# Kernel tuning notes

Measured on AMD Instinct MI355X. Metric: run time of the kernel, lower is better.

Reference implementation:

```python
import jax, jax.numpy as jnp
import numpy as np

B, T, D = 32, 2048, 256
HOUT, K = 512, 8
H = HOUT // 2  # per-direction hidden


def _lstm(x, w_ih, w_hh, b_ih, b_hh):
    # x: [B,T,D]; torch gate order i,f,g,o
    b = x.shape[0]
    h0 = jnp.zeros((b, H), x.dtype)
    c0 = jnp.zeros((b, H), x.dtype)
    def step(carry, x_t):
        h, c = carry
        g = x_t @ w_ih.T + b_ih + h @ w_hh.T + b_hh
        i, f, gg, o = jnp.split(g, 4, axis=-1)
        c = jax.nn.sigmoid(f) * c + jax.nn.sigmoid(i) * jnp.tanh(gg)
        h = jax.nn.sigmoid(o) * jnp.tanh(c)
        return (h, c), h
    _, hs = jax.lax.scan(step, (h0, c0), jnp.swapaxes(x, 0, 1))
    return jnp.swapaxes(hs, 0, 1)  # [B,T,H]


def setup_inputs() -> dict:
    key = jax.random.key(0)
    ks = jax.random.split(key, 16)
    s = 0.1
    lengths = jax.random.randint(ks[1], (B,), T // 2, T + 1)
    mask = (jnp.arange(T)[None, :] < lengths[:, None])
    inp = {
        "sentences": jax.random.normal(ks[0], (B, T, D), jnp.float32),
        "tags": jax.random.randint(ks[2], (B, T), 0, K),
        "lengths": lengths,
        "mask": mask,
        # forward-direction LSTM params
        "w_ih_f": jax.random.normal(ks[3], (4 * H, D), jnp.float32) * s,
        "w_hh_f": jax.random.normal(ks[4], (4 * H, H), jnp.float32) * s,
        "b_ih_f": jax.random.normal(ks[5], (4 * H,), jnp.float32) * s,
        "b_hh_f": jax.random.normal(ks[6], (4 * H,), jnp.float32) * s,
        # backward-direction LSTM params
        "w_ih_b": jax.random.normal(ks[7], (4 * H, D), jnp.float32) * s,
        "w_hh_b": jax.random.normal(ks[8], (4 * H, H), jnp.float32) * s,
        "b_ih_b": jax.random.normal(ks[9], (4 * H,), jnp.float32) * s,
        "b_hh_b": jax.random.normal(ks[10], (4 * H,), jnp.float32) * s,
        # hidden2tag linear
        "w_tag": jax.random.normal(ks[11], (K, HOUT), jnp.float32) * s,
        "b_tag": jax.random.normal(ks[12], (K,), jnp.float32) * s,
        # CRF params
        "start_trans": jax.random.normal(ks[13], (K,), jnp.float32) * s,
        "end_trans": jax.random.normal(ks[14], (K,), jnp.float32) * s,
        "trans": jax.random.normal(ks[15], (K, K), jnp.float32) * s,
    }
    return inp


def reference(sentences, tags, lengths, mask,
              w_ih_f, w_hh_f, b_ih_f, b_hh_f,
              w_ih_b, w_hh_b, b_ih_b, b_hh_b,
              w_tag, b_tag, start_trans, end_trans, trans):
    # --- BiLSTM features (dropout is identity at eval) ---
    t_idx = jnp.arange(T)[None, :]
    L = lengths[:, None]
    rev = jnp.where(t_idx < L, L - 1 - t_idx, t_idx)  # per-sequence reversal (involution)
    x_rev = jnp.take_along_axis(sentences, rev[:, :, None], axis=1)
    h_f = _lstm(sentences, w_ih_f, w_hh_f, b_ih_f, b_hh_f)
    h_b = jnp.take_along_axis(_lstm(x_rev, w_ih_b, w_hh_b, b_ih_b, b_hh_b), rev[:, :, None], axis=1)
    feats = jnp.concatenate([h_f, h_b], axis=-1)  # [B,T,HOUT]
    emis = feats @ w_tag.T + b_tag  # [B,T,K]

    m = mask.astype(emis.dtype)
    # --- CRF numerator (gold path score) ---
    tags0 = tags[:, 0]
    num = start_trans[tags0] + jnp.take_along_axis(emis[:, 0], tags0[:, None], 1)[:, 0]
    emis_tag = jnp.take_along_axis(emis, tags[:, :, None], 2)[..., 0]  # [B,T]
    tr = trans[tags[:, :-1], tags[:, 1:]]  # [B,T-1]
    num = num + jnp.sum((tr + emis_tag[:, 1:]) * m[:, 1:], axis=1)
    last_tags = jnp.take_along_axis(tags, (lengths - 1)[:, None], 1)[:, 0]
    num = num + end_trans[last_tags]

    # --- CRF log-partition (forward algorithm, logsumexp recurrence) ---
    def step(score, inp):
        e_t, m_t = inp  # [B,K], [B]
        nxt = jax.nn.logsumexp(score[:, :, None] + trans[None] + e_t[:, None, :], axis=1)
        return jnp.where(m_t[:, None], nxt, score), None
    score0 = start_trans[None, :] + emis[:, 0]
    xs = (jnp.swapaxes(emis[:, 1:], 0, 1), jnp.swapaxes(mask[:, 1:], 0, 1))
    scoreT, _ = jax.lax.scan(step, score0, xs)
    logZ = jax.nn.logsumexp(scoreT + end_trans[None, :], axis=1)

    # reduction='mean' log-likelihood, loss = -llh
    return -jnp.mean(num - logZ)
```

## Files before the change

kernel.cpp:

```cpp
#include <hip/hip_runtime.h>


constexpr int T_ = 2048, D_ = 256, K_ = 8;

typedef __bf16 v8bf __attribute__((ext_vector_type(8)));
typedef float  v4f  __attribute__((ext_vector_type(4)));
typedef int    v8i  __attribute__((ext_vector_type(8)));
typedef unsigned int u32;
typedef unsigned long long u64;

union U64x4 { u64 q[4]; v8i v; };

__device__ __forceinline__ float sigm(float x) {
  return __builtin_amdgcn_rcpf(1.f + __expf(-x));
}
__device__ __forceinline__ float tanh_f(float x) {
  return 1.f - 2.f * __builtin_amdgcn_rcpf(__expf(2.f * x) + 1.f);
}

__device__ __forceinline__ u32 pk2bf(float a, float b) {
  union { __bf16 h[2]; u32 u; } x; x.h[0] = (__bf16)a; x.h[1] = (__bf16)b; return x.u;
}
__device__ __forceinline__ float lobf(u32 u) { union { u32 u; __bf16 h[2]; } x; x.u = u; return (float)x.h[0]; }
__device__ __forceinline__ float hibf(u32 u) { union { u32 u; __bf16 h[2]; } x; x.u = u; return (float)x.h[1]; }

__device__ __forceinline__ int gate_row(int mtg, int rr) {
  return (rr & 3) * 256 + 32 * (mtg >> 3) + 8 * (rr >> 2) + (mtg & 7);
}


__global__ __launch_bounds__(256) void prepack(
    const float* __restrict__ w_hh_f, const float* __restrict__ w_hh_b,
    const float* __restrict__ b_ih_f, const float* __restrict__ b_hh_f,
    const float* __restrict__ b_ih_b, const float* __restrict__ b_hh_b,
    const float* __restrict__ w_tag,
    u64* wh8, v8bf* wt16, float* biasp, u32* hstate_u, float* cstate)
{
  int gid = blockIdx.x * 256 + threadIdx.x;
  if (gid < 65536) {
    int lane = gid & 63, kt = (gid >> 6) & 7, mtg = (gid >> 9) & 63, d = gid >> 15;
    int rr = lane & 15, q = lane >> 4;
    const float* whh = d ? w_hh_b : w_hh_f;
    const float* src = whh + (size_t)gate_row(mtg, rr) * 256
                           + 128 * (kt >> 2) + 32 * q + 8 * (kt & 3);
    u32 lo = __builtin_amdgcn_cvt_pk_fp8_f32(src[0], src[1], 0, false);
    lo = __builtin_amdgcn_cvt_pk_fp8_f32(src[2], src[3], lo, true);
    u32 hi = __builtin_amdgcn_cvt_pk_fp8_f32(src[4], src[5], 0, false);
    hi = __builtin_amdgcn_cvt_pk_fp8_f32(src[6], src[7], hi, true);
    wh8[gid] = ((u64)hi << 32) | lo;
  } else if (gid < 66560) {
    int g = gid - 65536;
    int lane = g & 63, kt = (g >> 6) & 7, d = (g >> 9) & 1;
    int rr = lane & 15, q = lane >> 4;
    v8bf v;
    #pragma unroll
    for (int e = 0; e < 8; ++e)
      v[e] = (rr < 8) ? (__bf16)w_tag[(size_t)rr * 512 + d * 256 + 32 * kt + 8 * q + e]
                      : (__bf16)0.f;
    wt16[g] = v;
  } else if (gid < 68608) {
    int g = gid - 66560;
    int p = g & 1023, d = g >> 10;
    int gr = gate_row(p >> 4, p & 15);
    biasp[g] = (d ? b_ih_b[gr] + b_hh_b[gr] : b_ih_f[gr] + b_hh_f[gr]);
  } else if (gid < 76800) {
    hstate_u[gid - 68608] = 0u;
  } else if (gid < 93184) {
    cstate[gid - 76800] = 0.f;
  }
}

__global__ __launch_bounds__(1024) void fused_chunk(
    const float* __restrict__ sent, const int* __restrict__ lengths,
    const float* __restrict__ w_ih_f, const float* __restrict__ w_ih_b,
    const float* __restrict__ biasp,
    const u64* __restrict__ wh8, const v8bf* __restrict__ wt16,
    __bf16* __restrict__ hstate, float* __restrict__ cstate,
    __bf16* __restrict__ pre, __bf16* __restrict__ hbuf,
    __bf16* __restrict__ emisF, __bf16* __restrict__ emisB,
    int crec, int cpre, int cemis, int CT, int TT, int nch, int NPREB)
{
  __shared__ __align__(16) char smem[33792];

  if (blockIdx.x < 4) {
    if (crec < 0) return;
    const int s = blockIdx.x, d = s >> 1, bg = s & 1;
    const int tid = threadIdx.x, lane = tid & 63, w = tid >> 6;
    const int fm = lane & 15, q = lane >> 4;
    const int e4 = 32 * (w >> 1) + 8 * q + 4 * (w & 1);
    int Lmax = 0;
    for (int i = 0; i < 32; ++i) Lmax = max(Lmax, lengths[i]);
    const int t0 = crec * CT, t1 = t0 + CT;
    const int tend = min(t1, Lmax);

    unsigned char* h8l = (unsigned char*)smem;

    {
      uint2 hv = *(const uint2*)(hstate + (size_t)s * 4096 + fm * 256 + e4);
      u32 pk8 = __builtin_amdgcn_cvt_pk_fp8_f32(lobf(hv.x), hibf(hv.x), 0, false);
      pk8 = __builtin_amdgcn_cvt_pk_fp8_f32(lobf(hv.y), hibf(hv.y), pk8, true);
      *(u32*)&h8l[4352 + fm * 272 + e4] = pk8;
    }

    v8i afr0[4], afr1[4];
    #pragma unroll
    for (int mt = 0; mt < 4; ++mt) {
      int mtg = 4 * w + mt;
      U64x4 lo, hi;
      #pragma unroll
      for (int jj = 0; jj < 4; ++jj) {
        lo.q[jj] = wh8[((size_t)(d * 64 + mtg) * 8 + jj) * 64 + lane];
        hi.q[jj] = wh8[((size_t)(d * 64 + mtg) * 8 + 4 + jj) * 64 + lane];
      }
      afr0[mt] = lo.v; afr1[mt] = hi.v;
    }
    float c8[4];
    #pragma unroll
    for (int mt = 0; mt < 4; ++mt) c8[mt] = cstate[((size_t)s * 1024 + tid) * 4 + mt];

    const char* preBase = (const char*)pre + (size_t)(crec & 1) * CT * 131072;
    __bf16* hslot = hbuf + ((size_t)(crec & 1) * 2 + d) * CT * 8192;
    const char* pb0 = preBase + (((size_t)d * CT * 32 + (bg * 16 + fm)) * 1024
                                 + 16 * (4 * w) + 4 * q) * 2;

    uint2 pA[4];
    #pragma unroll
    for (int mt = 0; mt < 4; ++mt)
      pA[mt] = *(const uint2*)(pb0 + 32 * mt);

    for (int t = t0; t < tend; ++t) {
      asm volatile("s_waitcnt lgkmcnt(0)" ::: "memory");
      __builtin_amdgcn_s_barrier();

      const int pp = (t + 1) & 1;
      v8i b0 = *(const v8i*)&h8l[pp * 4352 + fm * 272 + 32 * q];
      v8i b1 = *(const v8i*)&h8l[pp * 4352 + fm * 272 + 128 + 32 * q];

      v4f acc[4], accb[4];
      #pragma unroll
      for (int mt = 0; mt < 4; ++mt) {
        acc[mt] = v4f{lobf(pA[mt].x), hibf(pA[mt].x), lobf(pA[mt].y), hibf(pA[mt].y)};
        accb[mt] = v4f{0.f, 0.f, 0.f, 0.f};
      }

      {
        int tn = min(t + 1, tend - 1);
        const char* pb = pb0 + (size_t)(tn - t0) * 65536;
        #pragma unroll
        for (int mt = 0; mt < 4; ++mt)
          pA[mt] = *(const uint2*)(pb + 32 * mt);
      }

      #pragma unroll
      for (int mt = 0; mt < 4; ++mt)
        acc[mt] = __builtin_amdgcn_mfma_scale_f32_16x16x128_f8f6f4(
            afr0[mt], b0, acc[mt], 0, 0, 0, 0x7f7f7f7f, 0, 0x7f7f7f7f);
      #pragma unroll
      for (int mt = 0; mt < 4; ++mt)
        accb[mt] = __builtin_amdgcn_mfma_scale_f32_16x16x128_f8f6f4(
            afr1[mt], b1, accb[mt], 0, 0, 0, 0x7f7f7f7f, 0, 0x7f7f7f7f);

      float hh[4];
      #pragma unroll
      for (int mt = 0; mt < 4; ++mt) {
        float gi = acc[mt][0] + accb[mt][0];
        float gf = acc[mt][1] + accb[mt][1];
        float gg = acc[mt][2] + accb[mt][2];
        float go = acc[mt][3] + accb[mt][3];
        float c = sigm(gf) * c8[mt] + sigm(gi) * tanh_f(gg);
        c8[mt] = c;
        hh[mt] = sigm(go) * tanh_f(c);
      }

      {
        u32 pk8 = __builtin_amdgcn_cvt_pk_fp8_f32(hh[0], hh[1], 0, false);
        pk8 = __builtin_amdgcn_cvt_pk_fp8_f32(hh[2], hh[3], pk8, true);
        *(u32*)&h8l[(t & 1) * 4352 + fm * 272 + e4] = pk8;
      }
      {
        uint2 hv;
        hv.x = pk2bf(hh[0], hh[1]); hv.y = pk2bf(hh[2], hh[3]);
        *(uint2*)(hslot + ((size_t)(t - t0) * 32 + bg * 16 + fm) * 256 + e4) = hv;
        if (t == tend - 1)
          *(uint2*)(hstate + (size_t)s * 4096 + fm * 256 + e4) = hv;
      }
    }

    if (tend > t0) {
      #pragma unroll
      for (int mt = 0; mt < 4; ++mt) cstate[((size_t)s * 1024 + tid) * 4 + mt] = c8[mt];
    }
    return;
  }

  if ((int)blockIdx.x < 4 + NPREB) {
    if (cpre >= nch) return;
    const bool act = threadIdx.x < 512;
    const int u = (blockIdx.x - 4) * 2 + (threadIdx.x >> 8);
    const int b = u & 31, d = (u >> 5) & 1, zz = u >> 6;
    const int tg = zz >> 2, rg = zz & 3;
    const int tid = threadIdx.x & 255, lane = tid & 63, w = tid >> 6;
    const int fm = lane & 15, q = lane >> 4;
    const int NT = TT >> 4;
    const int t0 = cpre * CT;
    const float* wih = d ? w_ih_b : w_ih_f;
    __bf16* xl = (__bf16*)(smem + (threadIdx.x >> 8) * 16896);
    __bf16* preS = pre + (size_t)(cpre & 1) * CT * 65536;

    if (act) {
      const int Lb = lengths[b];
      for (int rep = 0; rep < NT; ++rep) {
        int tl = (tid >> 4) + 16 * rep, c16 = (tid & 15) * 16;
        int tglob = t0 + TT * tg + tl;
        int pos = d ? ((tglob < Lb) ? (Lb - 1 - tglob) : tglob) : tglob;
        const float4* xp = (const float4*)(sent + ((size_t)b * T_ + pos) * D_ + c16);
        float4 a0 = xp[0], a1 = xp[1], a2 = xp[2], a3 = xp[3];
        v8bf v0, v1;
        v0[0]=(__bf16)a0.x; v0[1]=(__bf16)a0.y; v0[2]=(__bf16)a0.z; v0[3]=(__bf16)a0.w;
        v0[4]=(__bf16)a1.x; v0[5]=(__bf16)a1.y; v0[6]=(__bf16)a1.z; v0[7]=(__bf16)a1.w;
        v1[0]=(__bf16)a2.x; v1[1]=(__bf16)a2.y; v1[2]=(__bf16)a2.z; v1[3]=(__bf16)a2.w;
        v1[4]=(__bf16)a3.x; v1[5]=(__bf16)a3.y; v1[6]=(__bf16)a3.z; v1[7]=(__bf16)a3.w;
        *(v8bf*)&xl[tl * 264 + c16]     = v0;
        *(v8bf*)&xl[tl * 264 + c16 + 8] = v1;
      }
    }
    __syncthreads();
    if (!act) return;

    v4f acc[4][2];
    #pragma unroll
    for (int mt = 0; mt < 4; ++mt) {
      float4 bs = *(const float4*)(biasp + d * 1024 + 16 * (16 * rg + 4 * w + mt) + 4 * q);
      for (int nt = 0; nt < 2; ++nt) acc[mt][nt] = v4f{bs.x, bs.y, bs.z, bs.w};
    }

    for (int kt = 0; kt < 8; ++kt) {
      v8bf af[4];
      #pragma unroll
      for (int mt = 0; mt < 4; ++mt) {
        const float* src = wih + (size_t)gate_row(16 * rg + 4 * w + mt, fm) * 256 + 8 * q + 32 * kt;
        float4 a = *(const float4*)(src);
        float4 b2 = *(const float4*)(src + 4);
        v8bf v;
        v[0]=(__bf16)a.x;  v[1]=(__bf16)a.y;  v[2]=(__bf16)a.z;  v[3]=(__bf16)a.w;
        v[4]=(__bf16)b2.x; v[5]=(__bf16)b2.y; v[6]=(__bf16)b2.z; v[7]=(__bf16)b2.w;
        af[mt] = v;
      }
      for (int nt = 0; nt < NT; ++nt) {
        v8bf bfr = *(const v8bf*)&xl[(nt * 16 + fm) * 264 + 32 * kt + 8 * q];
        #pragma unroll
        for (int mt = 0; mt < 4; ++mt)
          acc[mt][nt] = __builtin_amdgcn_mfma_f32_16x16x32_bf16(af[mt], bfr, acc[mt][nt], 0, 0, 0);
      }
    }

    #pragma unroll
    for (int mt = 0; mt < 4; ++mt) {
      int mtg = 16 * rg + 4 * w + mt;
      for (int nt = 0; nt < NT; ++nt) {
        int tl = TT * tg + nt * 16 + fm;
        uint2 pk;
        pk.x = pk2bf(acc[mt][nt][0], acc[mt][nt][1]);
        pk.y = pk2bf(acc[mt][nt][2], acc[mt][nt][3]);
        size_t off = (((size_t)d * CT + tl) * 32 + b) * 1024 + 16 * mtg + 4 * q;
        *(uint2*)((char*)preS + off * 2) = pk;
      }
    }
    return;
  }

  if (cemis < 0) return;
  {
    const int eb = blockIdx.x - 4 - NPREB;
    const int u = eb * 16 + (threadIdx.x >> 6);
    const int b = u & 31, d2 = (u >> 5) & 1, tg2 = u >> 6;
    if (tg2 >= CT / 16) return;
    const int lane = threadIdx.x & 63, fm = lane & 15, q = lane >> 4;
    const int Ln = lengths[b];
    const int tl = tg2 * 16 + fm;
    const __bf16* hrow = hbuf + ((((size_t)(cemis & 1) * 2 + d2) * CT + tl) * 32 + b) * 256;
    v4f ea = {0.f, 0.f, 0.f, 0.f};
    #pragma unroll
    for (int kt = 0; kt < 8; ++kt) {
      v8bf wa = wt16[((size_t)d2 * 8 + kt) * 64 + lane];
      v8bf hb = *(const v8bf*)(hrow + 32 * kt + 8 * q);
      ea = __builtin_amdgcn_mfma_f32_16x16x32_bf16(wa, hb, ea, 0, 0, 0);
    }
    int se = cemis * CT + tl;
    if (q < 2 && se < Ln) {
      int pos = d2 ? (Ln - 1 - se) : se;
      __bf16* emis = d2 ? emisB : emisF;
      uint2 pk; pk.x = pk2bf(ea[0], ea[1]); pk.y = pk2bf(ea[2], ea[3]);
      *(uint2*)((char*)emis + (((size_t)b * T_ + pos) * K_ + 4 * q) * 2) = pk;
    }
  }
}

__global__ __launch_bounds__(64) void crf_pass(
    const int* __restrict__ lengths, const int* __restrict__ tags,
    const float* __restrict__ b_tag, const float* __restrict__ start_trans,
    const float* __restrict__ end_trans, const float* __restrict__ trans,
    const __bf16* __restrict__ emisF, const __bf16* __restrict__ emisB, float* out)
{
  int b = blockIdx.x;
  int l = threadIdx.x;
  int L = lengths[b];
  int j = l >> 3, k = l & 7;
  float trl = trans[j * 8 + k];
  float btk = b_tag[k];
  const __bf16* eF = emisF + (size_t)b * T_ * K_;
  const __bf16* eB = emisB + (size_t)b * T_ * K_;
  const uint4* pF = (const uint4*)eF;
  const uint4* pB = (const uint4*)eB;

  __shared__ float buf[2][64][16];
  {
    uint4 uF = pF[l], uB = pB[l];
    float* r = &buf[0][l][0];
    r[0]=lobf(uF.x); r[1]=hibf(uF.x); r[2]=lobf(uF.y); r[3]=hibf(uF.y);
    r[4]=lobf(uF.z); r[5]=hibf(uF.z); r[6]=lobf(uF.w); r[7]=hibf(uF.w);
    r[8]=lobf(uB.x); r[9]=hibf(uB.x); r[10]=lobf(uB.y); r[11]=hibf(uB.y);
    r[12]=lobf(uB.z); r[13]=hibf(uB.z); r[14]=lobf(uB.w); r[15]=hibf(uB.w);
  }
  __syncthreads();

  float score = start_trans[j] + buf[0][0][j] + buf[0][0][8 + j] + b_tag[j];
  int nch = (L + 63) >> 6;
  for (int c = 0; c < nch; ++c) {
    uint4 preF, preB;
    bool more = (c + 1 < nch);
    if (more) { preF = pF[64 * (c + 1) + l]; preB = pB[64 * (c + 1) + l]; }
    int cur = c & 1;
    int tendc = min(64, L - 64 * c);
    for (int tt = (c == 0 ? 1 : 0); tt < tendc; ++tt) {
      float e = buf[cur][tt][k] + buf[cur][tt][8 + k] + btk;
      float m = __shfl(score, 0);
      float p = __expf(score + trl - m);
      p += __shfl_xor(p, 8); p += __shfl_xor(p, 16); p += __shfl_xor(p, 32);
      score = __shfl(m + __logf(p) + e, j);
    }
    if (more) {
      __syncthreads();
      float* r = &buf[cur ^ 1][l][0];
      r[0]=lobf(preF.x); r[1]=hibf(preF.x); r[2]=lobf(preF.y); r[3]=hibf(preF.y);
      r[4]=lobf(preF.z); r[5]=hibf(preF.z); r[6]=lobf(preF.w); r[7]=hibf(preF.w);
      r[8]=lobf(preB.x); r[9]=hibf(preB.x); r[10]=lobf(preB.y); r[11]=hibf(preB.y);
      r[12]=lobf(preB.z); r[13]=hibf(preB.z); r[14]=lobf(preB.w); r[15]=hibf(preB.w);
      __syncthreads();
    }
  }

  float v = score + end_trans[j];
  float m = fmaxf(v, __shfl_xor(v, 8)); m = fmaxf(m, __shfl_xor(m, 16)); m = fmaxf(m, __shfl_xor(m, 32));
  float p = __expf(v - m);
  p += __shfl_xor(p, 8); p += __shfl_xor(p, 16); p += __shfl_xor(p, 32);
  float logZ = m + __logf(p);

  const int* tg = tags + (size_t)b * T_;
  float nsum = 0.f;
  for (int t = l; t < L; t += 64) {
    int tt = tg[t];
    float e = (float)eF[t * 8 + tt] + (float)eB[t * 8 + tt] + b_tag[tt];
    float tr = (t > 0) ? trans[tg[t - 1] * 8 + tt] : 0.f;
    nsum += e + tr;
  }
  nsum += __shfl_xor(nsum, 1);  nsum += __shfl_xor(nsum, 2);  nsum += __shfl_xor(nsum, 4);
  nsum += __shfl_xor(nsum, 8);  nsum += __shfl_xor(nsum, 16); nsum += __shfl_xor(nsum, 32);
  if (l == 0) {
    float num = nsum + start_trans[tg[0]] + end_trans[tg[L - 1]];
    atomicAdd(out, (logZ - num) * (1.f / 32.f));
  }
}

extern "C" void kernel_launch(void* const* d_in, const int* in_sizes, int n_in,
                              void* d_out, int out_size, void* d_ws, size_t ws_size,
                              hipStream_t stream) {
  (void)in_sizes; (void)n_in; (void)out_size;
  const float* sent        = (const float*)d_in[0];
  const int*   tags        = (const int*)d_in[1];
  const int*   lengths     = (const int*)d_in[2];
  const float* w_ih_f      = (const float*)d_in[4];
  const float* w_hh_f      = (const float*)d_in[5];
  const float* b_ih_f      = (const float*)d_in[6];
  const float* b_hh_f      = (const float*)d_in[7];
  const float* w_ih_b      = (const float*)d_in[8];
  const float* w_hh_b      = (const float*)d_in[9];
  const float* b_ih_b      = (const float*)d_in[10];
  const float* b_hh_b      = (const float*)d_in[11];
  const float* w_tag       = (const float*)d_in[12];
  const float* b_tag       = (const float*)d_in[13];
  const float* start_trans = (const float*)d_in[14];
  const float* end_trans   = (const float*)d_in[15];
  const float* trans       = (const float*)d_in[16];

  char* ws = (char*)d_ws;
  u64*    wh8    = (u64*)(ws + 0x000000);
  v8bf*   wt16   = (v8bf*)(ws + 0x080000);
  float*  biasp  = (float*)(ws + 0x084000);
  __bf16* hstate = (__bf16*)(ws + 0x086000);
  float*  cstate = (float*)(ws + 0x08E000);
  __bf16* emisF  = (__bf16*)(ws + 0x100000);
  __bf16* emisB  = (__bf16*)(ws + 0x200000);
  __bf16* pre    = (__bf16*)(ws + 0x300000);

  int CT = 64;
  for (int cand : {256, 128}) {
    if ((size_t)0x300000 + (size_t)cand * (2 * 131072 + 2 * 32768) <= ws_size) { CT = cand; break; }
  }
  __bf16* hbuf = (__bf16*)(ws + 0x300000 + 2ull * (size_t)CT * 131072ull);
  const int TT = 32;
  const int nch = T_ / CT;
  const int NPREB = 128 * (CT / TT);
  const int NEMIS = CT / 4;
  dim3 grid(4 + NPREB + NEMIS, 1, 1);

  hipMemsetAsync(d_out, 0, sizeof(float), stream);
  prepack<<<364, 256, 0, stream>>>(w_hh_f, w_hh_b, b_ih_f, b_hh_f, b_ih_b, b_hh_b,
                                   w_tag, wh8, wt16, biasp, (u32*)hstate, cstate);
  fused_chunk<<<grid, 1024, 0, stream>>>(sent, lengths, w_ih_f, w_ih_b, biasp, wh8, wt16,
                                         hstate, cstate, pre, hbuf, emisF, emisB,
                                         -1, 0, -1, CT, TT, nch, NPREB);
  for (int c = 0; c < nch; ++c)
    fused_chunk<<<grid, 1024, 0, stream>>>(sent, lengths, w_ih_f, w_ih_b, biasp, wh8, wt16,
                                           hstate, cstate, pre, hbuf, emisF, emisB,
                                           c, c + 1, c - 1, CT, TT, nch, NPREB);
  fused_chunk<<<grid, 1024, 0, stream>>>(sent, lengths, w_ih_f, w_ih_b, biasp, wh8, wt16,
                                         hstate, cstate, pre, hbuf, emisF, emisB,
                                         -1, nch, nch - 1, CT, TT, nch, NPREB);
  crf_pass<<<32, 64, 0, stream>>>(lengths, tags, b_tag, start_trans, end_trans, trans,
                                  emisF, emisB, (float*)d_out);
}
```

Baseline: 4.440 ms.

## Split each LSTM recurrence across two workgroups exchanging fp8 hidden state via global flags

```diff
diff --git a/kernel.cpp b/kernel.cpp
--- a/kernel.cpp
+++ b/kernel.cpp
@@ -34,7 +34,7 @@
     const float* __restrict__ b_ih_f, const float* __restrict__ b_hh_f,
     const float* __restrict__ b_ih_b, const float* __restrict__ b_hh_b,
     const float* __restrict__ w_tag,
-    u64* wh8, v8bf* wt16, float* biasp, u32* hstate_u, float* cstate)
+    u64* wh8, v8bf* wt16, float* biasp, u32* zeroreg)
 {
   int gid = blockIdx.x * 256 + threadIdx.x;
   if (gid < 65536) {
@@ -63,10 +63,8 @@
     int p = g & 1023, d = g >> 10;
     int gr = gate_row(p >> 4, p & 15);
     biasp[g] = (d ? b_ih_b[gr] + b_hh_b[gr] : b_ih_f[gr] + b_hh_f[gr]);
-  } else if (gid < 76800) {
-    hstate_u[gid - 68608] = 0u;
-  } else if (gid < 93184) {
-    cstate[gid - 76800] = 0.f;
+  } else if (gid < 95232) {
+    zeroreg[gid - 68608] = 0u;
   }
 }
 
@@ -75,37 +73,44 @@
     const float* __restrict__ w_ih_f, const float* __restrict__ w_ih_b,
     const float* __restrict__ biasp,
     const u64* __restrict__ wh8, const v8bf* __restrict__ wt16,
-    __bf16* __restrict__ hstate, float* __restrict__ cstate,
+    u32* __restrict__ flags, unsigned char* __restrict__ mail,
+    float* __restrict__ cstate,
     __bf16* __restrict__ pre, __bf16* __restrict__ hbuf,
     __bf16* __restrict__ emisF, __bf16* __restrict__ emisB,
     int crec, int cpre, int cemis, int CT, int TT, int nch, int NPREB)
 {
   __shared__ __align__(16) char smem[33792];
 
-  if (blockIdx.x < 4) {
+  if (blockIdx.x < 16) {
     if (crec < 0) return;
-    const int s = blockIdx.x, d = s >> 1, bg = s & 1;
+    const int bid = blockIdx.x;
+    if (bid & 4) return;
+    const int db = bid & 3, half = bid >> 3, d = db >> 1, bg = db & 1;
     const int tid = threadIdx.x, lane = tid & 63, w = tid >> 6;
     const int fm = lane & 15, q = lane >> 4;
-    const int e4 = 32 * (w >> 1) + 8 * q + 4 * (w & 1);
+    const int e2 = 32 * (w >> 2) + 8 * q + ((2 * w) & 6);
+    const int mtg0 = 32 * half + 2 * w;
     int Lmax = 0;
     for (int i = 0; i < 32; ++i) Lmax = max(Lmax, lengths[i]);
-    const int t0 = crec * CT, t1 = t0 + CT;
-    const int tend = min(t1, Lmax);
+    const int t0 = crec * CT;
+    const int tend = min(t0 + CT, Lmax);
+    if (tend <= t0) return;
 
     unsigned char* h8l = (unsigned char*)smem;
 
-    {
-      uint2 hv = *(const uint2*)(hstate + (size_t)s * 4096 + fm * 256 + e4);
-      u32 pk8 = __builtin_amdgcn_cvt_pk_fp8_f32(lobf(hv.x), hibf(hv.x), 0, false);
-      pk8 = __builtin_amdgcn_cvt_pk_fp8_f32(lobf(hv.y), hibf(hv.y), pk8, true);
-      *(u32*)&h8l[4352 + fm * 272 + e4] = pk8;
-    }
-
-    v8i afr0[4], afr1[4];
-    #pragma unroll
-    for (int mt = 0; mt < 4; ++mt) {
-      int mtg = 4 * w + mt;
+    u32* fl_own[2] = { &flags[((db * 2 + 0) * 2 + half) * 16],
+                       &flags[((db * 2 + 1) * 2 + half) * 16] };
+    u32* fl_par[2] = { &flags[((db * 2 + 0) * 2 + (half ^ 1)) * 16],
+                       &flags[((db * 2 + 1) * 2 + (half ^ 1)) * 16] };
+    unsigned char* m_own[2] = { mail + (size_t)((db * 2 + 0) * 2 + half) * 2048,
+                                mail + (size_t)((db * 2 + 1) * 2 + half) * 2048 };
+    const unsigned char* m_par[2] = { mail + (size_t)((db * 2 + 0) * 2 + (half ^ 1)) * 2048,
+                                      mail + (size_t)((db * 2 + 1) * 2 + (half ^ 1)) * 2048 };
+
+    v8i afr0[2], afr1[2];
+    #pragma unroll
+    for (int mt = 0; mt < 2; ++mt) {
+      int mtg = mtg0 + mt;
       U64x4 lo, hi;
       #pragma unroll
       for (int jj = 0; jj < 4; ++jj) {
@@ -114,55 +119,68 @@
       }
       afr0[mt] = lo.v; afr1[mt] = hi.v;
     }
-    float c8[4];
-    #pragma unroll
-    for (int mt = 0; mt < 4; ++mt) c8[mt] = cstate[((size_t)s * 1024 + tid) * 4 + mt];
+    float c8[2];
+    #pragma unroll
+    for (int mt = 0; mt < 2; ++mt)
+      c8[mt] = cstate[((size_t)(db * 2 + half) * 1024 + tid) * 2 + mt];
 
     const char* preBase = (const char*)pre + (size_t)(crec & 1) * CT * 131072;
     __bf16* hslot = hbuf + ((size_t)(crec & 1) * 2 + d) * CT * 8192;
     const char* pb0 = preBase + (((size_t)d * CT * 32 + (bg * 16 + fm)) * 1024
-                                 + 16 * (4 * w) + 4 * q) * 2;
-
-    uint2 pA[4];
-    #pragma unroll
-    for (int mt = 0; mt < 4; ++mt)
-      pA[mt] = *(const uint2*)(pb0 + 32 * mt);
+                                 + 16 * mtg0 + 4 * q) * 2;
+
+    uint2 pA[2];
+    #pragma unroll
+    for (int mt = 0; mt < 2; ++mt) pA[mt] = *(const uint2*)(pb0 + 32 * mt);
+
+    {
+      unsigned short hv = *(const unsigned short*)(m_own[1] + fm * 128 + e2);
+      *(unsigned short*)&h8l[2176 + fm * 136 + e2] = hv;
+    }
+    __syncthreads();
 
     for (int t = t0; t < tend; ++t) {
-      asm volatile("s_waitcnt lgkmcnt(0)" ::: "memory");
-      __builtin_amdgcn_s_barrier();
-
       const int pp = (t + 1) & 1;
-      v8i b0 = *(const v8i*)&h8l[pp * 4352 + fm * 272 + 32 * q];
-      v8i b1 = *(const v8i*)&h8l[pp * 4352 + fm * 272 + 128 + 32 * q];
-
-      v4f acc[4], accb[4];
-      #pragma unroll
-      for (int mt = 0; mt < 4; ++mt) {
+      {
+        u32 v = __hip_atomic_load(fl_par[pp], __ATOMIC_ACQUIRE, __HIP_MEMORY_SCOPE_AGENT);
+        if ((int)v < t) {
+          for (int it = 0; it < (1 << 14); ++it) {
+            v = __hip_atomic_load(fl_par[pp], __ATOMIC_ACQUIRE, __HIP_MEMORY_SCOPE_AGENT);
+            if ((int)v >= t) break;
+            __builtin_amdgcn_s_sleep(2);
+          }
+        }
+      }
+      v8i bp = *(const v8i*)(m_par[pp] + fm * 128 + 32 * q);
+      v8i bo = *(const v8i*)&h8l[pp * 2176 + fm * 136 + 32 * q];
+
+      v4f acc[2], accb[2];
+      #pragma unroll
+      for (int mt = 0; mt < 2; ++mt) {
         acc[mt] = v4f{lobf(pA[mt].x), hibf(pA[mt].x), lobf(pA[mt].y), hibf(pA[mt].y)};
         accb[mt] = v4f{0.f, 0.f, 0.f, 0.f};
       }
-
       {
         int tn = min(t + 1, tend - 1);
         const char* pb = pb0 + (size_t)(tn - t0) * 65536;
         #pragma unroll
-        for (int mt = 0; mt < 4; ++mt)
-          pA[mt] = *(const uint2*)(pb + 32 * mt);
-      }
-
-      #pragma unroll
-      for (int mt = 0; mt < 4; ++mt)
+        for (int mt = 0; mt < 2; ++mt) pA[mt] = *(const uint2*)(pb + 32 * mt);
+      }
+
+      v8i bLO = half ? bp : bo;
+      v8i bHI = half ? bo : bp;
+      #pragma unroll
+      for (int mt = 0; mt < 2; ++mt)
         acc[mt] = __builtin_amdgcn_mfma_scale_f32_16x16x128_f8f6f4(
-            afr0[mt], b0, acc[mt], 0, 0, 0, 0x7f7f7f7f, 0, 0x7f7f7f7f);
-      #pragma unroll
-      for (int mt = 0; mt < 4; ++mt)
+            afr0[mt], bLO, acc[mt], 0, 0, 0, 0x7f7f7f7f, 0, 0x7f7f7f7f);
+      #pragma unroll
+      for (int mt = 0; mt < 2; ++mt)
         accb[mt] = __builtin_amdgcn_mfma_scale_f32_16x16x128_f8f6f4(
-            afr1[mt], b1, accb[mt], 0, 0, 0, 0x7f7f7f7f, 0, 0x7f7f7f7f);
-
-      float hh[4];
-      #pragma unroll
-      for (int mt = 0; mt < 4; ++mt) {
+            afr1[mt], bHI, accb[mt], 0, 0, 0, 0x7f7f7f7f, 0, 0x7f7f7f7f);
+
+      float hh[2];
+      #pragma unroll
+      for (int mt = 0; mt < 2; ++mt) {
         float gi = acc[mt][0] + accb[mt][0];
         float gf = acc[mt][1] + accb[mt][1];
         float gg = acc[mt][2] + accb[mt][2];
@@ -172,31 +190,29 @@
         hh[mt] = sigm(go) * tanh_f(c);
       }
 
-      {
-        u32 pk8 = __builtin_amdgcn_cvt_pk_fp8_f32(hh[0], hh[1], 0, false);
-        pk8 = __builtin_amdgcn_cvt_pk_fp8_f32(hh[2], hh[3], pk8, true);
-        *(u32*)&h8l[(t & 1) * 4352 + fm * 272 + e4] = pk8;
-      }
-      {
-        uint2 hv;
-        hv.x = pk2bf(hh[0], hh[1]); hv.y = pk2bf(hh[2], hh[3]);
-        *(uint2*)(hslot + ((size_t)(t - t0) * 32 + bg * 16 + fm) * 256 + e4) = hv;
-        if (t == tend - 1)
-          *(uint2*)(hstate + (size_t)s * 4096 + fm * 256 + e4) = hv;
-      }
-    }
-
-    if (tend > t0) {
-      #pragma unroll
-      for (int mt = 0; mt < 4; ++mt) cstate[((size_t)s * 1024 + tid) * 4 + mt] = c8[mt];
-    }
+      u32 pk8 = __builtin_amdgcn_cvt_pk_fp8_f32(hh[0], hh[1], 0, false);
+      *(unsigned short*)&h8l[(t & 1) * 2176 + fm * 136 + e2] = (unsigned short)pk8;
+      *(unsigned short*)(m_own[t & 1] + fm * 128 + e2) = (unsigned short)pk8;
+      *(u32*)(hslot + ((size_t)(t - t0) * 32 + bg * 16 + fm) * 256 + 128 * half + e2)
+          = pk2bf(hh[0], hh[1]);
+
+      asm volatile("s_waitcnt vmcnt(0) lgkmcnt(0)" ::: "memory");
+      __builtin_amdgcn_s_barrier();
+      if (tid == 0)
+        __hip_atomic_store(fl_own[t & 1], (u32)(t + 1), __ATOMIC_RELEASE,
+                           __HIP_MEMORY_SCOPE_AGENT);
+    }
+
+    #pragma unroll
+    for (int mt = 0; mt < 2; ++mt)
+      cstate[((size_t)(db * 2 + half) * 1024 + tid) * 2 + mt] = c8[mt];
     return;
   }
 
-  if ((int)blockIdx.x < 4 + NPREB) {
+  if ((int)blockIdx.x < 16 + NPREB) {
     if (cpre >= nch) return;
     const bool act = threadIdx.x < 512;
-    const int u = (blockIdx.x - 4) * 2 + (threadIdx.x >> 8);
+    const int u = (blockIdx.x - 16) * 2 + (threadIdx.x >> 8);
     const int b = u & 31, d = (u >> 5) & 1, zz = u >> 6;
     const int tg = zz >> 2, rg = zz & 3;
     const int tid = threadIdx.x & 255, lane = tid & 63, w = tid >> 6;
@@ -271,7 +287,7 @@
 
   if (cemis < 0) return;
   {
-    const int eb = blockIdx.x - 4 - NPREB;
+    const int eb = blockIdx.x - 16 - NPREB;
     const int u = eb * 16 + (threadIdx.x >> 6);
     const int b = u & 31, d2 = (u >> 5) & 1, tg2 = u >> 6;
     if (tg2 >= CT / 16) return;
@@ -397,8 +413,9 @@
   u64*    wh8    = (u64*)(ws + 0x000000);
   v8bf*   wt16   = (v8bf*)(ws + 0x080000);
   float*  biasp  = (float*)(ws + 0x084000);
-  __bf16* hstate = (__bf16*)(ws + 0x086000);
-  float*  cstate = (float*)(ws + 0x08E000);
+  u32*    flags  = (u32*)(ws + 0x086000);
+  unsigned char* mail = (unsigned char*)(ws + 0x088000);
+  float*  cstate = (float*)(ws + 0x090000);
   __bf16* emisF  = (__bf16*)(ws + 0x100000);
   __bf16* emisB  = (__bf16*)(ws + 0x200000);
   __bf16* pre    = (__bf16*)(ws + 0x300000);
@@ -412,20 +429,20 @@
   const int nch = T_ / CT;
   const int NPREB = 128 * (CT / TT);
   const int NEMIS = CT / 4;
-  dim3 grid(4 + NPREB + NEMIS, 1, 1);
+  dim3 grid(16 + NPREB + NEMIS, 1, 1);
 
   hipMemsetAsync(d_out, 0, sizeof(float), stream);
-  prepack<<<364, 256, 0, stream>>>(w_hh_f, w_hh_b, b_ih_f, b_hh_f, b_ih_b, b_hh_b,
-                                   w_tag, wh8, wt16, biasp, (u32*)hstate, cstate);
+  prepack<<<372, 256, 0, stream>>>(w_hh_f, w_hh_b, b_ih_f, b_hh_f, b_ih_b, b_hh_b,
+                                   w_tag, wh8, wt16, biasp, flags);
   fused_chunk<<<grid, 1024, 0, stream>>>(sent, lengths, w_ih_f, w_ih_b, biasp, wh8, wt16,
-                                         hstate, cstate, pre, hbuf, emisF, emisB,
+                                         flags, mail, cstate, pre, hbuf, emisF, emisB,
                                          -1, 0, -1, CT, TT, nch, NPREB);
   for (int c = 0; c < nch; ++c)
     fused_chunk<<<grid, 1024, 0, stream>>>(sent, lengths, w_ih_f, w_ih_b, biasp, wh8, wt16,
-                                           hstate, cstate, pre, hbuf, emisF, emisB,
+                                           flags, mail, cstate, pre, hbuf, emisF, emisB,
                                            c, c + 1, c - 1, CT, TT, nch, NPREB);
   fused_chunk<<<grid, 1024, 0, stream>>>(sent, lengths, w_ih_f, w_ih_b, biasp, wh8, wt16,
-                                         hstate, cstate, pre, hbuf, emisF, emisB,
+                                         flags, mail, cstate, pre, hbuf, emisF, emisB,
                                          -1, nch, nch - 1, CT, TT, nch, NPREB);
   crf_pass<<<32, 64, 0, stream>>>(lengths, tags, b_tag, start_trans, end_trans, trans,
                                   emisF, emisB, (float*)d_out);
```

After: 13.32 ms. 200% more time.
